# Performance work log

Measured on AMD Instinct MI355X. Metric: run time of the kernel, lower is better.

The kernel has to match this reference:

```python
import jax, jax.numpy as jnp
import numpy as np

N_NODES = 50000
N_EDGES = 800000
N_GRAPHS = 64
IN_DIM = 128
HID = 128
S, C = 4, 16
DIM1 = 3 * S * S  # 48
OUT_DIM = DIM1 * C  # 768


def gcn_conv(x, W, b, src, dst, w):
    """PyG GCNConv: linear transform, then sym-normalized aggregation with self-loops (weight 1)."""
    n = x.shape[0]
    h = x @ W  # [N, out]
    deg = jnp.zeros((n,), x.dtype).at[dst].add(w) + 1.0  # self-loop weight 1
    dinv = jax.lax.rsqrt(deg)
    norm = dinv[src] * w * dinv[dst]  # [E]
    agg = jnp.zeros_like(h).at[dst].add(h[src] * norm[:, None])
    agg = agg + h * (1.0 / deg)[:, None]  # self-loop messages
    return agg + b


def setup_inputs() -> dict:
    key = jax.random.key(0)
    ks = jax.random.split(key, 16)
    x = jax.random.normal(ks[0], (N_NODES, IN_DIM), jnp.float32)
    edge_index = jax.random.randint(ks[1], (2, N_EDGES), 0, N_NODES, jnp.int64)
    edge_attr = jax.random.uniform(ks[2], (N_EDGES,), jnp.float32)
    batch = jnp.sort(jax.random.randint(ks[3], (N_NODES,), 0, N_GRAPHS, jnp.int64))

    def glorot(k, fan_in, fan_out):
        s = np.sqrt(6.0 / (fan_in + fan_out)).astype(np.float32)
        return jax.random.uniform(k, (fan_in, fan_out), jnp.float32, -s, s)

    return {
        "x": x, "edge_index": edge_index, "edge_attr": edge_attr, "batch": batch,
        "W1": glorot(ks[4], IN_DIM, HID), "b1": jnp.zeros((HID,), jnp.float32),
        "W2": glorot(ks[5], HID, HID // 2), "b2": jnp.zeros((HID // 2,), jnp.float32),
        "W3": glorot(ks[6], HID // 2, HID // 4), "b3": jnp.zeros((HID // 4,), jnp.float32),
        "Wl": glorot(ks[7], HID // 4, OUT_DIM), "bl": jnp.zeros((OUT_DIM,), jnp.float32),
    }


def reference(x, edge_index, edge_attr, batch, W1, b1, W2, b2, W3, b3, Wl, bl):
    src, dst = edge_index[0], edge_index[1]
    w = edge_attr / edge_attr.max()
    h = jax.nn.relu(gcn_conv(x, W1, b1, src, dst, w))
    h = jax.nn.relu(gcn_conv(h, W2, b2, src, dst, w))
    h = jax.nn.relu(gcn_conv(h, W3, b3, src, dst, w))
    # global mean pool over graphs
    sums = jax.ops.segment_sum(h, batch, num_segments=N_GRAPHS)
    cnt = jax.ops.segment_sum(jnp.ones((h.shape[0],), h.dtype), batch, num_segments=N_GRAPHS)
    pooled = sums / jnp.maximum(cnt, 1.0)[:, None]
    out = pooled @ Wl + bl  # [G, OUT_DIM]
    return out.reshape(N_GRAPHS, DIM1, C)
```

## Files before the change

kernel.cpp:

```cpp
#include <hip/hip_runtime.h>
#include <hip/hip_bf16.h>

#define NN 50000
#define NE 800000
#define NG 64
#define OUTD 768

#define G1B ((NN + 63) / 64)
#define MAXB 128
#define SSEG 32
#define TTL 4
#define ESEG (NE / SSEG)
#define NTL (NN / TTL)
#define HRB (SSEG * TTL)

__device__ __forceinline__ float bflo(unsigned int u) { return __uint_as_float(u << 16); }
__device__ __forceinline__ float bfhi(unsigned int u) { return __uint_as_float(u & 0xffff0000u); }
__device__ __forceinline__ unsigned short f2bf(float f) {
    unsigned int u = __float_as_uint(f);
    return (unsigned short)((u + 0x7fffu + ((u >> 16) & 1u)) >> 16);
}
__device__ __forceinline__ unsigned int pack2bf(float lo, float hi) {
    return (unsigned int)f2bf(lo) | ((unsigned int)f2bf(hi) << 16);
}

typedef __attribute__((ext_vector_type(8))) short bf16x8;
typedef __attribute__((ext_vector_type(4))) float f32x4;
union FragU { uint4 u4; bf16x8 v; };

template <int K, int N>
constexpr int mfma_lds_bytes() { return (K / 32) * (N / 16) * 1024; }

template <int K, int N, typename TX>
__device__ __forceinline__ void mfma_gemm_body(char* smem,
                                               const TX* __restrict__ X,
                                               const float* __restrict__ W,
                                               unsigned short* __restrict__ Y,
                                               int nRows, int bx) {
    constexpr int NCT = N / 16;
    constexpr int KS = K / 32;
    const int tid = threadIdx.x;

    for (int q = tid; q < KS * NCT * 64; q += 256) {
        int lane = q & 63;
        int fi = q >> 6;
        int ct = fi % NCT, kc = fi / NCT;
        int col = ct * 16 + (lane & 15);
        int kb = kc * 32 + ((lane >> 4) << 3);
        uint4 w;
        w.x = pack2bf(W[(size_t)(kb + 0) * N + col], W[(size_t)(kb + 1) * N + col]);
        w.y = pack2bf(W[(size_t)(kb + 2) * N + col], W[(size_t)(kb + 3) * N + col]);
        w.z = pack2bf(W[(size_t)(kb + 4) * N + col], W[(size_t)(kb + 5) * N + col]);
        w.w = pack2bf(W[(size_t)(kb + 6) * N + col], W[(size_t)(kb + 7) * N + col]);
        *(uint4*)(smem + (size_t)q * 16) = w;
    }
    __syncthreads();

    const int lane = tid & 63;
    const int wv = tid >> 6;
    const int m = lane & 15;
    const int quad = lane >> 4;
    const int row = bx * 64 + wv * 16 + m;
    const bool rowok = row < nRows;
    const TX* xr = X + (size_t)(rowok ? row : 0) * K;

    f32x4 acc[NCT];
#pragma unroll
    for (int ct = 0; ct < NCT; ++ct) acc[ct] = (f32x4){0.f, 0.f, 0.f, 0.f};

#pragma unroll
    for (int kc = 0; kc < KS; ++kc) {
        const int k0 = kc * 32 + quad * 8;
        FragU a;
        if constexpr (sizeof(TX) == 4) {
            float4 a0 = make_float4(0.f, 0.f, 0.f, 0.f), a1 = a0;
            if (rowok) {
                a0 = *(const float4*)(xr + k0);
                a1 = *(const float4*)(xr + k0 + 4);
            }
            a.u4 = make_uint4(pack2bf(a0.x, a0.y), pack2bf(a0.z, a0.w),
                              pack2bf(a1.x, a1.y), pack2bf(a1.z, a1.w));
        } else {
            a.u4 = rowok ? *(const uint4*)(xr + k0) : make_uint4(0, 0, 0, 0);
        }
#pragma unroll
        for (int ct = 0; ct < NCT; ++ct) {
            FragU b;
            b.u4 = *(const uint4*)(smem + ((size_t)(kc * NCT + ct) * 64 + lane) * 16);
            acc[ct] = __builtin_amdgcn_mfma_f32_16x16x32_bf16(a.v, b.v, acc[ct], 0, 0, 0);
        }
    }

    const int orowb = bx * 64 + wv * 16 + quad * 4;
#pragma unroll
    for (int ct = 0; ct < NCT; ++ct) {
        int col = ct * 16 + m;
#pragma unroll
        for (int r = 0; r < 4; ++r) {
            int orow = orowb + r;
            if (orow < nRows) Y[(size_t)orow * N + col] = f2bf(acc[ct][r]);
        }
    }
}

template <int K, int N, typename TX>
__global__ __launch_bounds__(256) void mfma_gemm_kernel(const TX* __restrict__ X,
                                                        const float* __restrict__ W,
                                                        unsigned short* __restrict__ Y,
                                                        int nRows) {
    extern __shared__ char smem[];
    mfma_gemm_body<K, N>(smem, X, W, Y, nRows, blockIdx.x);
}

__global__ __launch_bounds__(256) void fused1_kernel(const float* __restrict__ x,
                                                     const float* __restrict__ W1,
                                                     unsigned short* __restrict__ bufA,
                                                     const float* __restrict__ ea,
                                                     unsigned int* wmax,
                                                     const int* __restrict__ dst,
                                                     int* __restrict__ rank,
                                                     unsigned short* __restrict__ pcnt) {
    extern __shared__ char smem[];
    const int b = blockIdx.x;
    if (b < G1B) {
        mfma_gemm_body<128, 128>(smem, x, W1, bufA, NN, b);
    } else if (b < G1B + MAXB) {
        float* red = (float*)smem;
        const int bb = b - G1B;
        const float4* ea4 = (const float4*)ea;
        float m = 0.0f;
        for (int i = bb * 256 + threadIdx.x; i < NE / 4; i += MAXB * 256) {
            float4 v = ea4[i];
            m = fmaxf(fmaxf(m, fmaxf(v.x, v.y)), fmaxf(v.z, v.w));
        }
        red[threadIdx.x] = m;
        __syncthreads();
        for (int off = 128; off > 0; off >>= 1) {
            if (threadIdx.x < off)
                red[threadIdx.x] = fmaxf(red[threadIdx.x], red[threadIdx.x + off]);
            __syncthreads();
        }
        if (threadIdx.x == 0) atomicMax(wmax, __float_as_uint(red[0]));
    } else {
        const int b2 = b - G1B - MAXB;
        const int seg = b2 >> 2;
        const int tile = b2 & 3;
        unsigned int* lcnt = (unsigned int*)smem;
        for (int i = threadIdx.x; i < NTL / 2; i += 256) lcnt[i] = 0;
        __syncthreads();
        const int base = seg * ESEG;
        const int nlo = tile * NTL;
        const int4* dst4 = (const int4*)(dst + base);
        for (int g = threadIdx.x; g < ESEG / 4; g += 256) {
            const int4 v = dst4[g];
            const int e0 = base + g * 4;
            const int dd[4] = {v.x, v.y, v.z, v.w};
#pragma unroll
            for (int j = 0; j < 4; ++j) {
                int d = dd[j] - nlo;
                if ((unsigned)d < (unsigned)NTL) {
                    unsigned sh = (unsigned)(d & 1) << 4;
                    unsigned old = atomicAdd(&lcnt[d >> 1], 1u << sh);
                    rank[e0 + j] = (int)((old >> sh) & 0xffffu);
                }
            }
        }
        __syncthreads();
        unsigned int* prow32 = (unsigned int*)(pcnt + (size_t)seg * NN + nlo);
        for (int i = threadIdx.x; i < NTL / 2; i += 256) prow32[i] = lcnt[i];
    }
}

__global__ __launch_bounds__(256) void comb_kernel(unsigned short* __restrict__ pcnt,
                                                   int* __restrict__ hist,
                                                   int* __restrict__ blocksum) {
    __shared__ int red[256];
    int n = blockIdx.x * 256 + threadIdx.x;
    int run = 0;
    if (n < NN) {
#pragma unroll
        for (int s = 0; s < SSEG; ++s) {
            size_t idx = (size_t)s * NN + n;
            int v = pcnt[idx];
            pcnt[idx] = (unsigned short)run;
            run += v;
        }
        hist[n] = run;
    }
    red[threadIdx.x] = (n < NN) ? run : 0;
    __syncthreads();
    for (int off = 128; off > 0; off >>= 1) {
        if (threadIdx.x < off) red[threadIdx.x] += red[threadIdx.x + off];
        __syncthreads();
    }
    if (threadIdx.x == 0) blocksum[blockIdx.x] = red[0];
}

__global__ __launch_bounds__(256) void scan3_kernel(const int* __restrict__ hist,
                                                    const int* __restrict__ blocksum,
                                                    int* __restrict__ rowptr, int n, int nb) {
    __shared__ int sb[256];
    __shared__ int s[256];
    const int tid = threadIdx.x;
    int bv = (tid < nb) ? blocksum[tid] : 0;
    sb[tid] = bv;
    __syncthreads();
    for (int off = 1; off < 256; off <<= 1) {
        int t = (tid >= off) ? sb[tid - off] : 0;
        __syncthreads();
        sb[tid] += t;
        __syncthreads();
    }
    const int boff = (blockIdx.x > 0) ? sb[blockIdx.x - 1] : 0;
    const int total = sb[nb - 1];

    int i = blockIdx.x * 256 + tid;
    int v = (i < n) ? hist[i] : 0;
    s[tid] = v;
    __syncthreads();
    for (int off = 1; off < 256; off <<= 1) {
        int t = (tid >= off) ? s[tid - off] : 0;
        __syncthreads();
        s[tid] += t;
        __syncthreads();
    }
    if (i < n) rowptr[i] = boff + s[tid] - v;
    if (blockIdx.x == 0 && tid == 0) rowptr[n] = total;
}

__global__ void scat_kernel(const int* __restrict__ src, const int* __restrict__ dst,
                            const float* __restrict__ ea,
                            const int* __restrict__ rowptr,
                            const unsigned short* __restrict__ pcnt,
                            const int* __restrict__ rank,
                            int2* __restrict__ epack, int nE) {
    int e = blockIdx.x * blockDim.x + threadIdx.x;
    if (e >= nE) return;
    int s = e / ESEG;
    int d = dst[e];
    int pos = rowptr[d] + (int)pcnt[(size_t)s * NN + d] + rank[e];
    epack[pos] = make_int2(src[e], __float_as_int(ea[e]));
}

__global__ void deg_kernel(const int2* __restrict__ epack, const int* __restrict__ rowptr,
                           const unsigned int* __restrict__ wmax,
                           float* __restrict__ nrm, float* __restrict__ invdeg, int n) {
    int i = blockIdx.x * blockDim.x + threadIdx.x;
    if (i >= n) return;
    float rw = 1.0f / __uint_as_float(*wmax);
    float srw = sqrtf(rw);
    int s0 = rowptr[i], s1 = rowptr[i + 1];
    float s = 0.f;
    for (int e = s0; e < s1; ++e) s += __int_as_float(epack[e].y);
    float d = fmaf(s, rw, 1.0f);
    nrm[i] = rsqrtf(d) * srw;
    invdeg[i] = 1.0f / d;
}

template <int D>
__global__ __launch_bounds__(256) void agg_kernel(const unsigned short* __restrict__ H,
                                                  const int* __restrict__ rowptr,
                                                  const int2* __restrict__ epack,
                                                  const float* __restrict__ invdeg,
                                                  const float* __restrict__ nrm,
                                                  const float* __restrict__ bias,
                                                  unsigned short* __restrict__ out,
                                                  int nNodes) {
    constexpr int LPE = D / 8;
    constexpr int EPW = 64 / LPE;
    const int lane = threadIdx.x & 63;
    const int n = (blockIdx.x << 2) | (threadIdx.x >> 6);
    if (n >= nNodes) return;
    const int esub = lane / LPE;
    const int f8 = (lane % LPE) * 8;
    const int s0 = rowptr[n];
    const int cnt = rowptr[n + 1] - s0;
    const float dn = nrm[n];

    float a[8] = {};
    int kb = 0;
    for (; kb + 2 * EPW <= cnt; kb += 2 * EPW) {
        const int2 pa = epack[s0 + kb + esub];
        const int2 pb = epack[s0 + kb + EPW + esub];
        const uint4 ua = *(const uint4*)(H + (size_t)pa.x * D + f8);
        const uint4 ub = *(const uint4*)(H + (size_t)pb.x * D + f8);
        const float ca = nrm[pa.x] * __int_as_float(pa.y) * dn;
        const float cb = nrm[pb.x] * __int_as_float(pb.y) * dn;
        a[0] = fmaf(ca, bflo(ua.x), a[0]); a[1] = fmaf(ca, bfhi(ua.x), a[1]);
        a[2] = fmaf(ca, bflo(ua.y), a[2]); a[3] = fmaf(ca, bfhi(ua.y), a[3]);
        a[4] = fmaf(ca, bflo(ua.z), a[4]); a[5] = fmaf(ca, bfhi(ua.z), a[5]);
        a[6] = fmaf(ca, bflo(ua.w), a[6]); a[7] = fmaf(ca, bfhi(ua.w), a[7]);
        a[0] = fmaf(cb, bflo(ub.x), a[0]); a[1] = fmaf(cb, bfhi(ub.x), a[1]);
        a[2] = fmaf(cb, bflo(ub.y), a[2]); a[3] = fmaf(cb, bfhi(ub.y), a[3]);
        a[4] = fmaf(cb, bflo(ub.z), a[4]); a[5] = fmaf(cb, bfhi(ub.z), a[5]);
        a[6] = fmaf(cb, bflo(ub.w), a[6]); a[7] = fmaf(cb, bfhi(ub.w), a[7]);
    }
    for (; kb < cnt; kb += EPW) {
        const int idx = kb + esub;
        const bool ok = idx < cnt;
        const int2 p = ok ? epack[s0 + idx] : make_int2(n, 0);
        const uint4 u = *(const uint4*)(H + (size_t)p.x * D + f8);
        const float c = ok ? nrm[p.x] * __int_as_float(p.y) * dn : 0.f;
        a[0] = fmaf(c, bflo(u.x), a[0]); a[1] = fmaf(c, bfhi(u.x), a[1]);
        a[2] = fmaf(c, bflo(u.y), a[2]); a[3] = fmaf(c, bfhi(u.y), a[3]);
        a[4] = fmaf(c, bflo(u.z), a[4]); a[5] = fmaf(c, bfhi(u.z), a[5]);
        a[6] = fmaf(c, bflo(u.w), a[6]); a[7] = fmaf(c, bfhi(u.w), a[7]);
    }
#pragma unroll
    for (int off = LPE; off < 64; off <<= 1) {
#pragma unroll
        for (int j = 0; j < 8; ++j) a[j] += __shfl_xor(a[j], off);
    }
    if (esub == 0) {
        const float id = invdeg[n];
        const uint4 un = *(const uint4*)(H + (size_t)n * D + f8);
        const float4 b0 = *(const float4*)(bias + f8);
        const float4 b1 = *(const float4*)(bias + f8 + 4);
        float o[8];
        o[0] = fmaxf(fmaf(id, bflo(un.x), a[0]) + b0.x, 0.f);
        o[1] = fmaxf(fmaf(id, bfhi(un.x), a[1]) + b0.y, 0.f);
        o[2] = fmaxf(fmaf(id, bflo(un.y), a[2]) + b0.z, 0.f);
        o[3] = fmaxf(fmaf(id, bfhi(un.y), a[3]) + b0.w, 0.f);
        o[4] = fmaxf(fmaf(id, bflo(un.z), a[4]) + b1.x, 0.f);
        o[5] = fmaxf(fmaf(id, bfhi(un.z), a[5]) + b1.y, 0.f);
        o[6] = fmaxf(fmaf(id, bflo(un.w), a[6]) + b1.z, 0.f);
        o[7] = fmaxf(fmaf(id, bfhi(un.w), a[7]) + b1.w, 0.f);
        uint4 w;
        w.x = pack2bf(o[0], o[1]);
        w.y = pack2bf(o[2], o[3]);
        w.z = pack2bf(o[4], o[5]);
        w.w = pack2bf(o[6], o[7]);
        *(uint4*)(out + (size_t)n * D + f8) = w;
    }
}

__global__ __launch_bounds__(256) void poolfin_kernel(const unsigned short* __restrict__ h,
                                                      const int* __restrict__ batch,
                                                      const float* __restrict__ Wl,
                                                      const float* __restrict__ bl,
                                                      float* __restrict__ out, int n) {
    const int g = blockIdx.x;
    int lo = 0, hi = n;
    while (lo < hi) { int m = (lo + hi) >> 1; if (batch[m] < g) lo = m + 1; else hi = m; }
    const int start = lo;
    lo = start; hi = n;
    while (lo < hi) { int m = (lo + hi) >> 1; if (batch[m] < g + 1) lo = m + 1; else hi = m; }
    const int end = lo;

    __shared__ float part[256];
    __shared__ float spool[32];
    const int f = threadIdx.x & 31;
    const int r = threadIdx.x >> 5;
    float acc = 0.f;
    for (int i = start + r; i < end; i += 8)
        acc += __uint_as_float((unsigned int)h[(size_t)i * 32 + f] << 16);
    part[threadIdx.x] = acc;
    __syncthreads();
    if (threadIdx.x < 32) {
        float s = 0.f;
#pragma unroll
        for (int q = 0; q < 8; ++q) s += part[q * 32 + f];
        float inv = 1.0f / fmaxf((float)(end - start), 1.0f);
        spool[f] = s * inv;
    }
    __syncthreads();
#pragma unroll
    for (int t = 0; t < 3; ++t) {
        const int o = t * 256 + threadIdx.x;
        float a2 = bl[o];
#pragma unroll
        for (int k = 0; k < 32; ++k)
            a2 = fmaf(spool[k], Wl[k * OUTD + o], a2);
        out[(size_t)g * OUTD + o] = a2;
    }
}

extern "C" void kernel_launch(void* const* d_in, const int* in_sizes, int n_in,
                              void* d_out, int out_size, void* d_ws, size_t ws_size,
                              hipStream_t stream) {
    const float* x = (const float*)d_in[0];
    const int* eidx = (const int*)d_in[1];
    const float* ea = (const float*)d_in[2];
    const int* batch = (const int*)d_in[3];
    const float* W1 = (const float*)d_in[4];
    const float* b1 = (const float*)d_in[5];
    const float* W2 = (const float*)d_in[6];
    const float* b2 = (const float*)d_in[7];
    const float* W3 = (const float*)d_in[8];
    const float* b3 = (const float*)d_in[9];
    const float* Wl = (const float*)d_in[10];
    const float* bl = (const float*)d_in[11];
    const int* src = eidx;
    const int* dst = eidx + NE;

    char* p = (char*)d_ws;
    auto take = [&](size_t bytes) {
        char* r = p;
        p += (bytes + 255) & ~(size_t)255;
        return r;
    };
    float* nrm = (float*)take(NN * 4);
    float* invdeg = (float*)take(NN * 4);
    int* hist = (int*)take(NN * 4);
    int* rowptr = (int*)take((NN + 1) * 4);
    int* blocksum = (int*)take(256 * 4);
    int2* epack = (int2*)take((size_t)NE * 8);
    unsigned int* wmax = (unsigned int*)take(4);
    unsigned short* bufA = (unsigned short*)take((size_t)NN * 128 * 2);
    unsigned short* bufB = (unsigned short*)take((size_t)NN * 128 * 2);
    int* rank = (int*)bufB;
    unsigned short* pcnt = (unsigned short*)((char*)bufB + (size_t)NE * 4 + 256);

    const int nblk = (NN + 255) / 256;
    const int eblk = (NE + 255) / 256;

    hipMemsetAsync(wmax, 0, 4, stream);

    constexpr int LDS1 = mfma_lds_bytes<128, 128>();
    static_assert(LDS1 >= NTL * 2, "HR branch LDS (packed u16 counters) must fit");
    fused1_kernel<<<G1B + MAXB + HRB, 256, LDS1, stream>>>(x, W1, bufA, ea, wmax,
                                                           dst, rank, pcnt);
    comb_kernel<<<nblk, 256, 0, stream>>>(pcnt, hist, blocksum);
    scan3_kernel<<<nblk, 256, 0, stream>>>(hist, blocksum, rowptr, NN, nblk);
    scat_kernel<<<eblk, 256, 0, stream>>>(src, dst, ea, rowptr, pcnt, rank, epack, NE);
    deg_kernel<<<nblk, 256, 0, stream>>>(epack, rowptr, wmax, nrm, invdeg, NN);

    agg_kernel<128><<<(NN + 3) / 4, 256, 0, stream>>>(bufA, rowptr, epack, invdeg, nrm, b1, bufB, NN);
    mfma_gemm_kernel<128, 64, unsigned short>
        <<<G1B, 256, mfma_lds_bytes<128, 64>(), stream>>>(bufB, W2, bufA, NN);
    agg_kernel<64><<<(NN + 3) / 4, 256, 0, stream>>>(bufA, rowptr, epack, invdeg, nrm, b2, bufB, NN);
    mfma_gemm_kernel<64, 32, unsigned short>
        <<<G1B, 256, mfma_lds_bytes<64, 32>(), stream>>>(bufB, W3, bufA, NN);
    agg_kernel<32><<<(NN + 7) / 8 * 2, 256, 0, stream>>>(bufA, rowptr, epack, invdeg, nrm, b3, bufB, NN);

    poolfin_kernel<<<NG, 256, 0, stream>>>(bufB, batch, Wl, bl, (float*)d_out, NN);
}
```

Before: 271.3 us.

## Replace segmented CSR build with global atomics and precompute edge coefficients

The multi-pass segmented histogram (per-segment LDS counters, combine pass) is replaced by global atomic counters and degree sums in the fused first kernel. This removes the comb and deg kernels. Per-edge normalization coefficients are now computed once during the scatter and stored in the edge pack, so the three aggregation passes no longer do gathered nrm lookups. The aggregation loop is unrolled to 4-edge batches, the 32-wide launch grid is changed, and pooling uses 1024-thread blocks. Global atomics add contention and make edge order within a row, and so the float summation order, nondeterministic.

```diff
diff --git a/kernel.cpp b/kernel.cpp
--- a/kernel.cpp
+++ b/kernel.cpp
@@ -7,12 +7,8 @@
 #define OUTD 768
 
 #define G1B ((NN + 63) / 64)
-#define MAXB 128
-#define SSEG 32
-#define TTL 4
-#define ESEG (NE / SSEG)
-#define NTL (NN / TTL)
-#define HRB (SSEG * TTL)
+#define HRB 250
+#define EHR (NE / HRB)
 
 __device__ __forceinline__ float bflo(unsigned int u) { return __uint_as_float(u << 16); }
 __device__ __forceinline__ float bfhi(unsigned int u) { return __uint_as_float(u & 0xffff0000u); }
@@ -119,75 +115,63 @@
                                                      unsigned int* wmax,
                                                      const int* __restrict__ dst,
                                                      int* __restrict__ rank,
-                                                     unsigned short* __restrict__ pcnt) {
+                                                     int* __restrict__ gcnt,
+                                                     float* __restrict__ dsum) {
     extern __shared__ char smem[];
     const int b = blockIdx.x;
     if (b < G1B) {
         mfma_gemm_body<128, 128>(smem, x, W1, bufA, NN, b);
-    } else if (b < G1B + MAXB) {
+    } else {
+        const int b2 = b - G1B;
+        const int base = b2 * EHR;
+        const int4* dst4 = (const int4*)(dst + base);
+        const float4* ea4 = (const float4*)(ea + base);
+        int4* rank4 = (int4*)(rank + base);
+        float m = 0.0f;
+        for (int g = threadIdx.x; g < EHR / 4; g += 256) {
+            const int4 dv = dst4[g];
+            const float4 ev = ea4[g];
+            int4 r;
+            r.x = atomicAdd(&gcnt[dv.x], 1);
+            r.y = atomicAdd(&gcnt[dv.y], 1);
+            r.z = atomicAdd(&gcnt[dv.z], 1);
+            r.w = atomicAdd(&gcnt[dv.w], 1);
+            atomicAdd(&dsum[dv.x], ev.x);
+            atomicAdd(&dsum[dv.y], ev.y);
+            atomicAdd(&dsum[dv.z], ev.z);
+            atomicAdd(&dsum[dv.w], ev.w);
+            m = fmaxf(fmaxf(m, fmaxf(ev.x, ev.y)), fmaxf(ev.z, ev.w));
+            rank4[g] = r;
+        }
+#pragma unroll
+        for (int off = 32; off > 0; off >>= 1) m = fmaxf(m, __shfl_xor(m, off));
         float* red = (float*)smem;
-        const int bb = b - G1B;
-        const float4* ea4 = (const float4*)ea;
-        float m = 0.0f;
-        for (int i = bb * 256 + threadIdx.x; i < NE / 4; i += MAXB * 256) {
-            float4 v = ea4[i];
-            m = fmaxf(fmaxf(m, fmaxf(v.x, v.y)), fmaxf(v.z, v.w));
+        if ((threadIdx.x & 63) == 0) red[threadIdx.x >> 6] = m;
+        __syncthreads();
+        if (threadIdx.x == 0) {
+            float mm = fmaxf(fmaxf(red[0], red[1]), fmaxf(red[2], red[3]));
+            atomicMax(wmax, __float_as_uint(mm));
         }
-        red[threadIdx.x] = m;
-        __syncthreads();
-        for (int off = 128; off > 0; off >>= 1) {
-            if (threadIdx.x < off)
-                red[threadIdx.x] = fmaxf(red[threadIdx.x], red[threadIdx.x + off]);
-            __syncthreads();
-        }
-        if (threadIdx.x == 0) atomicMax(wmax, __float_as_uint(red[0]));
-    } else {
-        const int b2 = b - G1B - MAXB;
-        const int seg = b2 >> 2;
-        const int tile = b2 & 3;
-        unsigned int* lcnt = (unsigned int*)smem;
-        for (int i = threadIdx.x; i < NTL / 2; i += 256) lcnt[i] = 0;
-        __syncthreads();
-        const int base = seg * ESEG;
-        const int nlo = tile * NTL;
-        const int4* dst4 = (const int4*)(dst + base);
-        for (int g = threadIdx.x; g < ESEG / 4; g += 256) {
-            const int4 v = dst4[g];
-            const int e0 = base + g * 4;
-            const int dd[4] = {v.x, v.y, v.z, v.w};
-#pragma unroll
-            for (int j = 0; j < 4; ++j) {
-                int d = dd[j] - nlo;
-                if ((unsigned)d < (unsigned)NTL) {
-                    unsigned sh = (unsigned)(d & 1) << 4;
-                    unsigned old = atomicAdd(&lcnt[d >> 1], 1u << sh);
-                    rank[e0 + j] = (int)((old >> sh) & 0xffffu);
-                }
-            }
-        }
-        __syncthreads();
-        unsigned int* prow32 = (unsigned int*)(pcnt + (size_t)seg * NN + nlo);
-        for (int i = threadIdx.x; i < NTL / 2; i += 256) prow32[i] = lcnt[i];
-    }
-}
-
-__global__ __launch_bounds__(256) void comb_kernel(unsigned short* __restrict__ pcnt,
-                                                   int* __restrict__ hist,
-                                                   int* __restrict__ blocksum) {
+    }
+}
+
+__global__ __launch_bounds__(256) void mid_kernel(const int* __restrict__ gcnt,
+                                                  const float* __restrict__ dsum,
+                                                  const unsigned int* __restrict__ wmax,
+                                                  int* __restrict__ blocksum,
+                                                  float* __restrict__ nrm,
+                                                  float* __restrict__ invdeg) {
     __shared__ int red[256];
-    int n = blockIdx.x * 256 + threadIdx.x;
-    int run = 0;
+    const int n = blockIdx.x * 256 + threadIdx.x;
+    int v = 0;
     if (n < NN) {
-#pragma unroll
-        for (int s = 0; s < SSEG; ++s) {
-            size_t idx = (size_t)s * NN + n;
-            int v = pcnt[idx];
-            pcnt[idx] = (unsigned short)run;
-            run += v;
-        }
-        hist[n] = run;
-    }
-    red[threadIdx.x] = (n < NN) ? run : 0;
+        v = gcnt[n];
+        float rw = 1.0f / __uint_as_float(*wmax);
+        float d = fmaf(dsum[n], rw, 1.0f);
+        nrm[n] = rsqrtf(d) * sqrtf(rw);
+        invdeg[n] = 1.0f / d;
+    }
+    red[threadIdx.x] = v;
     __syncthreads();
     for (int off = 128; off > 0; off >>= 1) {
         if (threadIdx.x < off) red[threadIdx.x] += red[threadIdx.x + off];
@@ -231,30 +215,16 @@
 __global__ void scat_kernel(const int* __restrict__ src, const int* __restrict__ dst,
                             const float* __restrict__ ea,
                             const int* __restrict__ rowptr,
-                            const unsigned short* __restrict__ pcnt,
                             const int* __restrict__ rank,
+                            const float* __restrict__ nrm,
                             int2* __restrict__ epack, int nE) {
     int e = blockIdx.x * blockDim.x + threadIdx.x;
     if (e >= nE) return;
-    int s = e / ESEG;
+    int s = e < nE ? src[e] : 0;
     int d = dst[e];
-    int pos = rowptr[d] + (int)pcnt[(size_t)s * NN + d] + rank[e];
-    epack[pos] = make_int2(src[e], __float_as_int(ea[e]));
-}
-
-__global__ void deg_kernel(const int2* __restrict__ epack, const int* __restrict__ rowptr,
-                           const unsigned int* __restrict__ wmax,
-                           float* __restrict__ nrm, float* __restrict__ invdeg, int n) {
-    int i = blockIdx.x * blockDim.x + threadIdx.x;
-    if (i >= n) return;
-    float rw = 1.0f / __uint_as_float(*wmax);
-    float srw = sqrtf(rw);
-    int s0 = rowptr[i], s1 = rowptr[i + 1];
-    float s = 0.f;
-    for (int e = s0; e < s1; ++e) s += __int_as_float(epack[e].y);
-    float d = fmaf(s, rw, 1.0f);
-    nrm[i] = rsqrtf(d) * srw;
-    invdeg[i] = 1.0f / d;
+    int pos = rowptr[d] + rank[e];
+    float coef = nrm[s] * ea[e] * nrm[d];
+    epack[pos] = make_int2(s, __float_as_int(coef));
 }
 
 template <int D>
@@ -262,7 +232,6 @@
                                                   const int* __restrict__ rowptr,
                                                   const int2* __restrict__ epack,
                                                   const float* __restrict__ invdeg,
-                                                  const float* __restrict__ nrm,
                                                   const float* __restrict__ bias,
                                                   unsigned short* __restrict__ out,
                                                   int nNodes) {
@@ -275,37 +244,49 @@
     const int f8 = (lane % LPE) * 8;
     const int s0 = rowptr[n];
     const int cnt = rowptr[n + 1] - s0;
-    const float dn = nrm[n];
+    const int2* ep = epack + s0;
 
     float a[8] = {};
+#define AGG8(c_, u_)                                                            \
+    a[0] = fmaf(c_, bflo(u_.x), a[0]); a[1] = fmaf(c_, bfhi(u_.x), a[1]);       \
+    a[2] = fmaf(c_, bflo(u_.y), a[2]); a[3] = fmaf(c_, bfhi(u_.y), a[3]);       \
+    a[4] = fmaf(c_, bflo(u_.z), a[4]); a[5] = fmaf(c_, bfhi(u_.z), a[5]);       \
+    a[6] = fmaf(c_, bflo(u_.w), a[6]); a[7] = fmaf(c_, bfhi(u_.w), a[7]);
+
     int kb = 0;
+    for (; kb + 4 * EPW <= cnt; kb += 4 * EPW) {
+        const int2 p0 = ep[kb + 0 * EPW + esub];
+        const int2 p1 = ep[kb + 1 * EPW + esub];
+        const int2 p2 = ep[kb + 2 * EPW + esub];
+        const int2 p3 = ep[kb + 3 * EPW + esub];
+        const uint4 u0 = *(const uint4*)(H + (size_t)p0.x * D + f8);
+        const uint4 u1 = *(const uint4*)(H + (size_t)p1.x * D + f8);
+        const uint4 u2 = *(const uint4*)(H + (size_t)p2.x * D + f8);
+        const uint4 u3 = *(const uint4*)(H + (size_t)p3.x * D + f8);
+        const float c0 = __int_as_float(p0.y);
+        const float c1 = __int_as_float(p1.y);
+        const float c2 = __int_as_float(p2.y);
+        const float c3 = __int_as_float(p3.y);
+        AGG8(c0, u0) AGG8(c1, u1) AGG8(c2, u2) AGG8(c3, u3)
+    }
     for (; kb + 2 * EPW <= cnt; kb += 2 * EPW) {
-        const int2 pa = epack[s0 + kb + esub];
-        const int2 pb = epack[s0 + kb + EPW + esub];
-        const uint4 ua = *(const uint4*)(H + (size_t)pa.x * D + f8);
-        const uint4 ub = *(const uint4*)(H + (size_t)pb.x * D + f8);
-        const float ca = nrm[pa.x] * __int_as_float(pa.y) * dn;
-        const float cb = nrm[pb.x] * __int_as_float(pb.y) * dn;
-        a[0] = fmaf(ca, bflo(ua.x), a[0]); a[1] = fmaf(ca, bfhi(ua.x), a[1]);
-        a[2] = fmaf(ca, bflo(ua.y), a[2]); a[3] = fmaf(ca, bfhi(ua.y), a[3]);
-        a[4] = fmaf(ca, bflo(ua.z), a[4]); a[5] = fmaf(ca, bfhi(ua.z), a[5]);
-        a[6] = fmaf(ca, bflo(ua.w), a[6]); a[7] = fmaf(ca, bfhi(ua.w), a[7]);
-        a[0] = fmaf(cb, bflo(ub.x), a[0]); a[1] = fmaf(cb, bfhi(ub.x), a[1]);
-        a[2] = fmaf(cb, bflo(ub.y), a[2]); a[3] = fmaf(cb, bfhi(ub.y), a[3]);
-        a[4] = fmaf(cb, bflo(ub.z), a[4]); a[5] = fmaf(cb, bfhi(ub.z), a[5]);
-        a[6] = fmaf(cb, bflo(ub.w), a[6]); a[7] = fmaf(cb, bfhi(ub.w), a[7]);
+        const int2 p0 = ep[kb + esub];
+        const int2 p1 = ep[kb + EPW + esub];
+        const uint4 u0 = *(const uint4*)(H + (size_t)p0.x * D + f8);
+        const uint4 u1 = *(const uint4*)(H + (size_t)p1.x * D + f8);
+        const float c0 = __int_as_float(p0.y);
+        const float c1 = __int_as_float(p1.y);
+        AGG8(c0, u0) AGG8(c1, u1)
     }
     for (; kb < cnt; kb += EPW) {
         const int idx = kb + esub;
         const bool ok = idx < cnt;
-        const int2 p = ok ? epack[s0 + idx] : make_int2(n, 0);
+        const int2 p = ok ? ep[idx] : make_int2(n, 0);
         const uint4 u = *(const uint4*)(H + (size_t)p.x * D + f8);
-        const float c = ok ? nrm[p.x] * __int_as_float(p.y) * dn : 0.f;
-        a[0] = fmaf(c, bflo(u.x), a[0]); a[1] = fmaf(c, bfhi(u.x), a[1]);
-        a[2] = fmaf(c, bflo(u.y), a[2]); a[3] = fmaf(c, bfhi(u.y), a[3]);
-        a[4] = fmaf(c, bflo(u.z), a[4]); a[5] = fmaf(c, bfhi(u.z), a[5]);
-        a[6] = fmaf(c, bflo(u.w), a[6]); a[7] = fmaf(c, bfhi(u.w), a[7]);
-    }
+        const float c = ok ? __int_as_float(p.y) : 0.f;
+        AGG8(c, u)
+    }
+#undef AGG8
 #pragma unroll
     for (int off = LPE; off < 64; off <<= 1) {
 #pragma unroll
@@ -334,11 +315,11 @@
     }
 }
 
-__global__ __launch_bounds__(256) void poolfin_kernel(const unsigned short* __restrict__ h,
-                                                      const int* __restrict__ batch,
-                                                      const float* __restrict__ Wl,
-                                                      const float* __restrict__ bl,
-                                                      float* __restrict__ out, int n) {
+__global__ __launch_bounds__(1024) void poolfin_kernel(const unsigned short* __restrict__ h,
+                                                       const int* __restrict__ batch,
+                                                       const float* __restrict__ Wl,
+                                                       const float* __restrict__ bl,
+                                                       float* __restrict__ out, int n) {
     const int g = blockIdx.x;
     int lo = 0, hi = n;
     while (lo < hi) { int m = (lo + hi) >> 1; if (batch[m] < g) lo = m + 1; else hi = m; }
@@ -347,26 +328,25 @@
     while (lo < hi) { int m = (lo + hi) >> 1; if (batch[m] < g + 1) lo = m + 1; else hi = m; }
     const int end = lo;
 
-    __shared__ float part[256];
+    __shared__ float part[1024];
     __shared__ float spool[32];
     const int f = threadIdx.x & 31;
     const int r = threadIdx.x >> 5;
     float acc = 0.f;
-    for (int i = start + r; i < end; i += 8)
+    for (int i = start + r; i < end; i += 32)
         acc += __uint_as_float((unsigned int)h[(size_t)i * 32 + f] << 16);
     part[threadIdx.x] = acc;
     __syncthreads();
     if (threadIdx.x < 32) {
         float s = 0.f;
 #pragma unroll
-        for (int q = 0; q < 8; ++q) s += part[q * 32 + f];
+        for (int q = 0; q < 32; ++q) s += part[q * 32 + f];
         float inv = 1.0f / fmaxf((float)(end - start), 1.0f);
         spool[f] = s * inv;
     }
     __syncthreads();
-#pragma unroll
-    for (int t = 0; t < 3; ++t) {
-        const int o = t * 256 + threadIdx.x;
+    if (threadIdx.x < OUTD) {
+        const int o = threadIdx.x;
         float a2 = bl[o];
 #pragma unroll
         for (int k = 0; k < 32; ++k)
@@ -401,37 +381,36 @@
     };
     float* nrm = (float*)take(NN * 4);
     float* invdeg = (float*)take(NN * 4);
-    int* hist = (int*)take(NN * 4);
     int* rowptr = (int*)take((NN + 1) * 4);
     int* blocksum = (int*)take(256 * 4);
     int2* epack = (int2*)take((size_t)NE * 8);
-    unsigned int* wmax = (unsigned int*)take(4);
+    char* zbase = take(NN * 4 + NN * 4 + 256);
+    int* gcnt = (int*)zbase;
+    float* dsum = (float*)(zbase + (size_t)NN * 4);
+    unsigned int* wmax = (unsigned int*)(zbase + (size_t)NN * 8);
     unsigned short* bufA = (unsigned short*)take((size_t)NN * 128 * 2);
     unsigned short* bufB = (unsigned short*)take((size_t)NN * 128 * 2);
     int* rank = (int*)bufB;
-    unsigned short* pcnt = (unsigned short*)((char*)bufB + (size_t)NE * 4 + 256);
 
     const int nblk = (NN + 255) / 256;
     const int eblk = (NE + 255) / 256;
 
-    hipMemsetAsync(wmax, 0, 4, stream);
+    hipMemsetAsync(zbase, 0, (size_t)NN * 8 + 4, stream);
 
     constexpr int LDS1 = mfma_lds_bytes<128, 128>();
-    static_assert(LDS1 >= NTL * 2, "HR branch LDS (packed u16 counters) must fit");
-    fused1_kernel<<<G1B + MAXB + HRB, 256, LDS1, stream>>>(x, W1, bufA, ea, wmax,
-                                                           dst, rank, pcnt);
-    comb_kernel<<<nblk, 256, 0, stream>>>(pcnt, hist, blocksum);
-    scan3_kernel<<<nblk, 256, 0, stream>>>(hist, blocksum, rowptr, NN, nblk);
-    scat_kernel<<<eblk, 256, 0, stream>>>(src, dst, ea, rowptr, pcnt, rank, epack, NE);
-    deg_kernel<<<nblk, 256, 0, stream>>>(epack, rowptr, wmax, nrm, invdeg, NN);
-
-    agg_kernel<128><<<(NN + 3) / 4, 256, 0, stream>>>(bufA, rowptr, epack, invdeg, nrm, b1, bufB, NN);
+    fused1_kernel<<<G1B + HRB, 256, LDS1, stream>>>(x, W1, bufA, ea, wmax,
+                                                    dst, rank, gcnt, dsum);
+    mid_kernel<<<nblk, 256, 0, stream>>>(gcnt, dsum, wmax, blocksum, nrm, invdeg);
+    scan3_kernel<<<nblk, 256, 0, stream>>>(gcnt, blocksum, rowptr, NN, nblk);
+    scat_kernel<<<eblk, 256, 0, stream>>>(src, dst, ea, rowptr, rank, nrm, epack, NE);
+
+    agg_kernel<128><<<(NN + 3) / 4, 256, 0, stream>>>(bufA, rowptr, epack, invdeg, b1, bufB, NN);
     mfma_gemm_kernel<128, 64, unsigned short>
         <<<G1B, 256, mfma_lds_bytes<128, 64>(), stream>>>(bufB, W2, bufA, NN);
-    agg_kernel<64><<<(NN + 3) / 4, 256, 0, stream>>>(bufA, rowptr, epack, invdeg, nrm, b2, bufB, NN);
+    agg_kernel<64><<<(NN + 3) / 4, 256, 0, stream>>>(bufA, rowptr, epack, invdeg, b2, bufB, NN);
     mfma_gemm_kernel<64, 32, unsigned short>
         <<<G1B, 256, mfma_lds_bytes<64, 32>(), stream>>>(bufB, W3, bufA, NN);
-    agg_kernel<32><<<(NN + 7) / 8 * 2, 256, 0, stream>>>(bufA, rowptr, epack, invdeg, nrm, b3, bufB, NN);
-
-    poolfin_kernel<<<NG, 256, 0, stream>>>(bufB, batch, Wl, bl, (float*)d_out, NN);
-}
+    agg_kernel<32><<<(NN + 3) / 4, 256, 0, stream>>>(bufA, rowptr, epack, invdeg, b3, bufB, NN);
+
+    poolfin_kernel<<<NG, 1024, 0, stream>>>(bufB, batch, Wl, bl, (float*)d_out, NN);
+}
```

Result: slower. 310.0 us (+14.3%).
